# Kernel optimization log

Measured on AMD Instinct MI355X. Metric: run time of the kernel, lower is better.

## Reference

```python
import jax, jax.numpy as jnp
import numpy as np

B, T, C, WD = 8, 2048, 768, 512
TD, CD = 384, 3072   # tokens_dim=0.5*C, channels_dim=4*C
H1 = C               # default hidden of token StyleGLUs
EPS = 1e-6


def _ln(x, g, b):
    mu = jnp.mean(x, -1, keepdims=True)
    v = jnp.mean((x - mu) ** 2, -1, keepdims=True)
    return (x - mu) * jax.lax.rsqrt(v + EPS) * g + b


def _style_glu(x, w, gW, gb, sW, sb, mW, mb):
    # gate linear -> GLU -> style-modulated matmul (modulation folded into einsum)
    h = x @ gW + gb                       # [B,T,H]
    a, gt = jnp.split(h, 2, axis=-1)
    a = a * jax.nn.sigmoid(gt)            # [B,T,H/2]
    s = w @ sW + sb                       # [B,H/2] per-sample style scale
    return jnp.einsum('bth,bh,ho->bto', a, s, mW) + mb


def setup_inputs() -> dict:
    key = jax.random.key(0)
    ks = iter(jax.random.split(key, 40))
    def nrm(*s, sc=0.02):
        return jax.random.normal(next(ks), s, dtype=jnp.float32) * sc
    return dict(
        x=jax.random.normal(next(ks), (B, T, C), dtype=jnp.float32),
        w=jax.random.normal(next(ks), (B, 2, WD), dtype=jnp.float32),
        ln1_g=jnp.ones(C, jnp.float32), ln1_b=jnp.zeros(C, jnp.float32),
        ln2_g=jnp.ones(C, jnp.float32), ln2_b=jnp.zeros(C, jnp.float32),
        g1_W=nrm(C, H1), g1_b=jnp.zeros(H1, jnp.float32),
        s1_W=nrm(WD, H1 // 2), s1_b=jnp.zeros(H1 // 2, jnp.float32),
        m1_W=nrm(H1 // 2, TD, sc=0.05), m1_b=nrm(TD, sc=0.05),
        g2_W=nrm(C, H1), g2_b=jnp.zeros(H1, jnp.float32),
        s2_W=nrm(WD, H1 // 2), s2_b=jnp.zeros(H1 // 2, jnp.float32),
        m2_W=nrm(H1 // 2, TD, sc=0.05), m2_b=nrm(TD, sc=0.05),
        gs_W=nrm(C, CD), gs_b=jnp.zeros(CD, jnp.float32),
        ss_W=nrm(WD, CD // 2), ss_b=jnp.zeros(CD // 2, jnp.float32),
        ms_W=nrm(CD // 2, C, sc=0.05), ms_b=nrm(C, sc=0.05),
        r1_W=nrm(C, C), r1_b=jnp.zeros(C, jnp.float32),
        r2_W=nrm(C // 2, C), r2_b=jnp.zeros(C, jnp.float32),
    )


def reference(x, w, ln1_g, ln1_b, ln2_g, ln2_b,
              g1_W, g1_b, s1_W, s1_b, m1_W, m1_b,
              g2_W, g2_b, s2_W, s2_b, m2_W, m2_b,
              gs_W, gs_b, ss_W, ss_b, ms_W, ms_b,
              r1_W, r1_b, r2_W, r2_b):
    x = _ln(x, ln1_g, ln1_b)
    w0, w1 = w[:, 0], w[:, 1]
    # --- StyleHyperMixer token mixing (eval: dropout/droppath = identity) ---
    h1 = _style_glu(x, w0, g1_W, g1_b, s1_W, s1_b, m1_W, m1_b)  # [B,T,TD]
    h2 = _style_glu(x, w0, g2_W, g2_b, s2_W, s2_b, m2_W, m2_b)  # [B,T,TD]
    mix = jax.nn.gelu(jnp.einsum('btd,btc->bdc', h1, x), approximate=False)  # [B,TD,C]
    x = x + jnp.einsum('btd,bdc->btc', h2, mix)
    # --- style-modulated channel MLP ---
    x = x + _style_glu(_ln(x, ln2_g, ln2_b), w1, gs_W, gs_b, ss_W, ss_b, ms_W, ms_b)
    # --- GLU reduce ---
    h = x @ r1_W + r1_b
    a, gt = jnp.split(h, 2, axis=-1)
    return (a * jax.nn.sigmoid(gt)) @ r2_W + r2_b
```

## Files before the change

kernel.cpp:

```cpp
#include <hip/hip_runtime.h>
#include <hip/hip_bf16.h>
#include <math.h>

#define NB 8
#define NT 2048
#define NC 768
#define ROWS (NB*NT)

typedef __attribute__((ext_vector_type(8))) short s8v;
typedef __attribute__((ext_vector_type(4))) float f4v;

__device__ __forceinline__ unsigned short f2b(float f) {
    unsigned u = __builtin_bit_cast(unsigned, f);
    return (unsigned short)((u + 0x7FFFu + ((u >> 16) & 1u)) >> 16);
}

__device__ __forceinline__ void gll16(const ushort* g, ushort* l) {
    __builtin_amdgcn_global_load_lds(
        (const __attribute__((address_space(1))) void*)g,
        (__attribute__((address_space(3))) void*)l, 16, 0, 0);
}

template<int N> __device__ __forceinline__ void waitcnt_vm() {
    if constexpr (N == 3)      asm volatile("s_waitcnt vmcnt(3)" ::: "memory");
    else if constexpr (N == 4) asm volatile("s_waitcnt vmcnt(4)" ::: "memory");
    else if constexpr (N == 6) asm volatile("s_waitcnt vmcnt(6)" ::: "memory");
    else                       asm volatile("s_waitcnt vmcnt(0)" ::: "memory");
}
__device__ __forceinline__ void hw_barrier() {
    asm volatile("s_barrier" ::: "memory");
}

template<int R>
__device__ __forceinline__ void stageL(ushort* __restrict__ L, const ushort* __restrict__ G,
                                       int ld, int r0, int k0, int lane, int w) {
    int rs = lane >> 2, c = lane & 3;
#pragma unroll
    for (int i = 0; i < R / 64; i++) {
        int ii = w + 4 * i;
        int row = ii * 16 + rs;
        int kc = (c ^ ((row >> 1) & 3)) << 3;
        gll16(G + (long)(r0 + row) * ld + k0 + kc, L + ii * 512);
    }
}

template<int TN, int EPI, bool HASBIAS, bool SPLITK>
__global__ __launch_bounds__(256) void gemm_mfma(
    const ushort* __restrict__ A, const ushort* __restrict__ Bt,
    float* __restrict__ Cf, ushort* __restrict__ Cb,
    int M, int N, int K, int lda, int ldb, int ldc,
    long sA, long sB, long sC, const float* __restrict__ bias)
{
    constexpr int WM = (TN == 128) ? 64 : 32;
    constexpr int TI = WM / 16;
    constexpr int BN = TN * 32;
    constexpr int LP = 2 + TN / 64;
    int zz = blockIdx.z;
    int z  = SPLITK ? (zz >> 2) : zz;
    int kb = SPLITK ? (zz & 3) * (K >> 2) : 0;
    int ke = SPLITK ? kb + (K >> 2) : K;
    const ushort* Az = A + (long)z * sA;
    const ushort* Bz = Bt + (long)z * sB;
    float*  Cfz = Cf ? Cf + (long)z * sC : nullptr;
    ushort* Cbz = Cb ? Cb + (long)z * sC : nullptr;

    int m0 = blockIdx.y * 128, n0 = blockIdx.x * TN;
    __shared__ alignas(16) ushort Al[8192];
    __shared__ alignas(16) ushort Bl[2 * BN];
    int t = threadIdx.x;
    int lane = t & 63, w = t >> 6;
    int wm = (TN == 128) ? (w >> 1) * 64 : w * 32;
    int wn = (TN == 128) ? (w & 1) * 64 : 0;
    int fr = lane & 15, q = lane >> 4;

    f4v acc[TI][4];
#pragma unroll
    for (int i = 0; i < TI; i++)
#pragma unroll
        for (int j = 0; j < 4; j++) acc[i][j] = (f4v)(0.0f);

    auto frag_mfma = [&](const ushort* AB, const ushort* BB) {
        s8v af[TI], bf[4];
#pragma unroll
        for (int ti = 0; ti < TI; ti++) {
            int r = wm + ti * 16 + fr;
            af[ti] = *(const s8v*)&AB[r * 32 + ((q ^ ((r >> 1) & 3)) << 3)];
        }
#pragma unroll
        for (int tj = 0; tj < 4; tj++) {
            int r = wn + tj * 16 + fr;
            bf[tj] = *(const s8v*)&BB[r * 32 + ((q ^ ((r >> 1) & 3)) << 3)];
        }
#pragma unroll
        for (int ti = 0; ti < TI; ti++)
#pragma unroll
            for (int tj = 0; tj < 4; tj++)
                acc[ti][tj] = __builtin_amdgcn_mfma_f32_16x16x32_bf16(
                    af[ti], bf[tj], acc[ti][tj], 0, 0, 0);
    };

    int nt = (ke - kb) >> 5;
    stageL<128>(Al, Az, lda, m0, kb, lane, w);
    stageL<TN>(Bl, Bz, ldb, n0, kb, lane, w);
    int cur = 0;
    for (int it = 0; it + 1 < nt; ++it) {
        stageL<128>(Al + (cur ^ 1) * 4096, Az, lda, m0, kb + (it + 1) * 32, lane, w);
        stageL<TN>(Bl + (cur ^ 1) * BN, Bz, ldb, n0, kb + (it + 1) * 32, lane, w);
        waitcnt_vm<LP>();
        hw_barrier();
        frag_mfma(Al + cur * 4096, Bl + cur * BN);
        hw_barrier();
        cur ^= 1;
    }
    waitcnt_vm<0>();
    hw_barrier();
    frag_mfma(Al + cur * 4096, Bl + cur * BN);

    int cr0 = q * 4;
#pragma unroll
    for (int ti = 0; ti < TI; ti++) {
#pragma unroll
        for (int tj = 0; tj < 4; tj++) {
            int n = n0 + wn + tj * 16 + fr;
            float bv = HASBIAS ? bias[n] : 0.0f;
#pragma unroll
            for (int r = 0; r < 4; r++) {
                int m = m0 + wm + ti * 16 + cr0 + r;
                long idx = (long)m * ldc + n;
                float v = acc[ti][tj][r] + bv;
                if (EPI == 0) {
                    Cbz[idx] = f2b(v);
                } else if (EPI == 5) {
                    Cfz[idx] = v;
                } else if (EPI == 6) {
                    __hip_atomic_fetch_add(&Cfz[idx], v, __ATOMIC_RELAXED,
                                           __HIP_MEMORY_SCOPE_AGENT);
                } else {
                    v += Cfz[idx];
                    if (EPI == 3) Cfz[idx] = v;
                    if (EPI == 4) Cbz[idx] = f2b(v);
                }
            }
        }
    }
}

template<int TN, bool HAS_S>
__global__ __launch_bounds__(256) void gemm_glu_mfma(
    const ushort* __restrict__ A,
    const ushort* __restrict__ Bt0, const ushort* __restrict__ Bt1,
    ushort* __restrict__ C0, ushort* __restrict__ C1,
    int M, int Nh, int K, int lda,
    const float* __restrict__ bias0, const float* __restrict__ bias1,
    const float* __restrict__ s0, const float* __restrict__ s1, int bofs)
{
    constexpr int WM = (TN == 128) ? 64 : 32;
    constexpr int TI = WM / 16;
    constexpr int BN = TN * 32;
    constexpr int LP = 2 + 2 * (TN / 64);
    int z = blockIdx.z;
    const ushort* Bt = z ? Bt1 : Bt0;
    ushort* Cb = z ? C1 : C0;
    const float* bias = z ? bias1 : bias0;
    const float* s = z ? s1 : s0;

    int m0 = blockIdx.y * 128, n0 = blockIdx.x * TN;
    __shared__ alignas(16) ushort Al[8192];
    __shared__ alignas(16) ushort B1[2 * BN];
    __shared__ alignas(16) ushort B2[2 * BN];
    int t = threadIdx.x;
    int lane = t & 63, w = t >> 6;
    int wm = (TN == 128) ? (w >> 1) * 64 : w * 32;
    int wn = (TN == 128) ? (w & 1) * 64 : 0;
    int fr = lane & 15, q = lane >> 4;

    f4v acc1[TI][4], acc2[TI][4];
#pragma unroll
    for (int i = 0; i < TI; i++)
#pragma unroll
        for (int j = 0; j < 4; j++) { acc1[i][j] = (f4v)(0.0f); acc2[i][j] = (f4v)(0.0f); }

    auto frag_mfma = [&](const ushort* AB, const ushort* BB1, const ushort* BB2) {
        s8v af[TI], b1f[4], b2f[4];
#pragma unroll
        for (int ti = 0; ti < TI; ti++) {
            int r = wm + ti * 16 + fr;
            af[ti] = *(const s8v*)&AB[r * 32 + ((q ^ ((r >> 1) & 3)) << 3)];
        }
#pragma unroll
        for (int tj = 0; tj < 4; tj++) {
            int r = wn + tj * 16 + fr;
            int o = r * 32 + ((q ^ ((r >> 1) & 3)) << 3);
            b1f[tj] = *(const s8v*)&BB1[o];
            b2f[tj] = *(const s8v*)&BB2[o];
        }
#pragma unroll
        for (int ti = 0; ti < TI; ti++)
#pragma unroll
            for (int tj = 0; tj < 4; tj++) {
                acc1[ti][tj] = __builtin_amdgcn_mfma_f32_16x16x32_bf16(af[ti], b1f[tj], acc1[ti][tj], 0, 0, 0);
                acc2[ti][tj] = __builtin_amdgcn_mfma_f32_16x16x32_bf16(af[ti], b2f[tj], acc2[ti][tj], 0, 0, 0);
            }
    };

    int nt = K >> 5;
    stageL<TN>(B1, Bt, K, n0, 0, lane, w);
    stageL<TN>(B2, Bt, K, Nh + n0, 0, lane, w);
    stageL<128>(Al, A, lda, m0, 0, lane, w);
    int cur = 0;
    for (int it = 0; it + 1 < nt; ++it) {
        int k0 = (it + 1) * 32;
        stageL<TN>(B1 + (cur ^ 1) * BN, Bt, K, n0, k0, lane, w);
        stageL<TN>(B2 + (cur ^ 1) * BN, Bt, K, Nh + n0, k0, lane, w);
        stageL<128>(Al + (cur ^ 1) * 4096, A, lda, m0, k0, lane, w);
        waitcnt_vm<LP>();
        hw_barrier();
        frag_mfma(Al + cur * 4096, B1 + cur * BN, B2 + cur * BN);
        hw_barrier();
        cur ^= 1;
    }
    waitcnt_vm<0>();
    hw_barrier();
    frag_mfma(Al + cur * 4096, B1 + cur * BN, B2 + cur * BN);

    int cr0 = q * 4;
#pragma unroll
    for (int ti = 0; ti < TI; ti++) {
        int bb = ((m0 + wm + ti * 16 + cr0) >> 11) + bofs;
#pragma unroll
        for (int tj = 0; tj < 4; tj++) {
            int n = n0 + wn + tj * 16 + fr;
            float bv = bias[n], bg = bias[Nh + n];
            float sv = HAS_S ? s[(long)bb * Nh + n] : 1.0f;
#pragma unroll
            for (int r = 0; r < 4; r++) {
                int m = m0 + wm + ti * 16 + cr0 + r;
                float vv = acc1[ti][tj][r] + bv;
                float gg = acc2[ti][tj][r] + bg;
                float a = vv * (1.0f / (1.0f + __expf(-gg)));
                if (HAS_S) a *= sv;
                Cb[(long)m * Nh + n] = f2b(a);
            }
        }
    }
}

__global__ __launch_bounds__(256) void gelu_cast_kernel(const float* __restrict__ in,
                                                        ushort* __restrict__ out) {
    int i4 = (blockIdx.x * 256 + threadIdx.x) * 4;
    float4 v = *(const float4*)(in + i4);
    ushort4 o;
    o.x = f2b(0.5f * v.x * (1.0f + erff(v.x * 0.70710678118654752440f)));
    o.y = f2b(0.5f * v.y * (1.0f + erff(v.y * 0.70710678118654752440f)));
    o.z = f2b(0.5f * v.z * (1.0f + erff(v.z * 0.70710678118654752440f)));
    o.w = f2b(0.5f * v.w * (1.0f + erff(v.w * 0.70710678118654752440f)));
    *(ushort4*)(out + i4) = o;
}

template<bool SRC_F32>
__global__ __launch_bounds__(256) void transpose_kernel(const void* __restrict__ src,
                                                        ushort* __restrict__ dst,
                                                        int R, int C, long sS, long sD) {
    int z = blockIdx.z;
    const void* S = SRC_F32 ? (const void*)((const float*)src + (long)z * sS)
                            : (const void*)((const ushort*)src + (long)z * sS);
    ushort* D = dst + (long)z * sD;
    int r0 = blockIdx.y * 64, c0 = blockIdx.x * 64;
    __shared__ ushort T[64][68];
    int t = threadIdx.x;
#pragma unroll
    for (int p = 0; p < 4; p++) {
        int e = p * 256 + t;
        int row = e >> 4, cc = (e & 15) * 4;
        ushort4 v;
        if (SRC_F32) {
            float4 f = *(const float4*)((const float*)S + (long)(r0 + row) * C + c0 + cc);
            v.x = f2b(f.x); v.y = f2b(f.y); v.z = f2b(f.z); v.w = f2b(f.w);
        } else {
            v = *(const ushort4*)((const ushort*)S + (long)(r0 + row) * C + c0 + cc);
        }
        *(ushort4*)&T[row][cc] = v;
    }
    __syncthreads();
#pragma unroll
    for (int p = 0; p < 4; p++) {
        int e = p * 256 + t;
        int crow = e >> 4, rr = (e & 15) * 4;
        ushort4 o;
        o.x = T[rr + 0][crow]; o.y = T[rr + 1][crow];
        o.z = T[rr + 2][crow]; o.w = T[rr + 3][crow];
        *(ushort4*)&D[(long)(c0 + crow) * R + r0 + rr] = o;
    }
}

__global__ __launch_bounds__(256) void prep_kernel(
    const float* __restrict__ g1_W, ushort* __restrict__ g1t,
    const float* __restrict__ g2_W, ushort* __restrict__ g2t,
    const float* __restrict__ m1_W, ushort* __restrict__ m1t,
    const float* __restrict__ m2_W, ushort* __restrict__ m2t,
    const float* __restrict__ gs_W, ushort* __restrict__ gst,
    const float* __restrict__ ms_W, ushort* __restrict__ mst,
    const float* __restrict__ r1_W, ushort* __restrict__ r1t,
    const float* __restrict__ r2_W, ushort* __restrict__ r2t,
    const float* __restrict__ w,
    const float* __restrict__ s1W, const float* __restrict__ s1b,
    const float* __restrict__ s2W, const float* __restrict__ s2b,
    const float* __restrict__ ssW, const float* __restrict__ ssb,
    float* __restrict__ sout)
{
    int b = blockIdx.x, t = threadIdx.x;
    if (b < 23040) {
        const float* W; ushort* Wt; int K, N, lo;
        if      (b < 2304)  { W = g1_W; Wt = g1t; K = 768;  N = 768;  lo = 0; }
        else if (b < 4608)  { W = g2_W; Wt = g2t; K = 768;  N = 768;  lo = 2304; }
        else if (b < 5184)  { W = m1_W; Wt = m1t; K = 384;  N = 384;  lo = 4608; }
        else if (b < 5760)  { W = m2_W; Wt = m2t; K = 384;  N = 384;  lo = 5184; }
        else if (b < 14976) { W = gs_W; Wt = gst; K = 768;  N = 3072; lo = 5760; }
        else if (b < 19584) { W = ms_W; Wt = mst; K = 1536; N = 768;  lo = 14976; }
        else if (b < 21888) { W = r1_W; Wt = r1t; K = 768;  N = 768;  lo = 19584; }
        else                { W = r2_W; Wt = r2t; K = 384;  N = 768;  lo = 21888; }
        int local = b - lo, bx = K >> 6;
        int byi = local / bx, bxi = local - byi * bx;
        int k = bxi * 64 + (t & 63), n = byi * 4 + (t >> 6);
        Wt[(long)n * K + k] = f2b(W[(long)k * N + n]);
    } else {
        int gid = (b - 23040) * 256 + t;
        int bb = gid / 2304;
        int r  = gid % 2304;
        const float* w0 = w + (long)bb * 1024;
        const float* w1 = w0 + 512;
        float acc = 0.f;
        if (r < 384) {
            for (int k = 0; k < 512; k++) acc += w0[k] * s1W[k * 384 + r];
            sout[bb * 384 + r] = acc + s1b[r];
        } else if (r < 768) {
            int c = r - 384;
            for (int k = 0; k < 512; k++) acc += w0[k] * s2W[k * 384 + c];
            sout[3072 + bb * 384 + c] = acc + s2b[c];
        } else {
            int c = r - 768;
            for (int k = 0; k < 512; k++) acc += w1[k] * ssW[k * 1536 + c];
            sout[6144 + bb * 1536 + c] = acc + ssb[c];
        }
    }
}

template<int MODE>
__global__ __launch_bounds__(256) void ln_kernel(const float* __restrict__ x,
                                                 const float* __restrict__ g,
                                                 const float* __restrict__ b,
                                                 float* __restrict__ outf,
                                                 ushort* __restrict__ outb) {
    int row = blockIdx.x;
    const float* xr = x + (long)row * NC;
    int t = threadIdx.x;
    float v0 = xr[t], v1 = xr[t + 256], v2 = xr[t + 512];
    float s = v0 + v1 + v2;
    float s2 = v0 * v0 + v1 * v1 + v2 * v2;
    for (int off = 32; off > 0; off >>= 1) {
        s  += __shfl_down(s, off, 64);
        s2 += __shfl_down(s2, off, 64);
    }
    __shared__ float ls[4], ls2[4];
    int wid = t >> 6, lane = t & 63;
    if (lane == 0) { ls[wid] = s; ls2[wid] = s2; }
    __syncthreads();
    if (t == 0) {
        float ts = ls[0] + ls[1] + ls[2] + ls[3];
        float ts2 = ls2[0] + ls2[1] + ls2[2] + ls2[3];
        float mu = ts * (1.0f / NC);
        float var = ts2 * (1.0f / NC) - mu * mu;
        ls[0] = mu;
        ls2[0] = 1.0f / sqrtf(var + 1e-6f);
    }
    __syncthreads();
    float mu = ls[0], r = ls2[0];
#pragma unroll
    for (int i = 0; i < 3; i++) {
        int c = t + i * 256;
        float vv = (i == 0 ? v0 : (i == 1 ? v1 : v2));
        float o = (vv - mu) * r * g[c] + b[c];
        if (MODE == 2) outf[(long)row * NC + c] = o;
        outb[(long)row * NC + c] = f2b(o);
    }
}

extern "C" void kernel_launch(void* const* d_in, const int* in_sizes, int n_in,
                              void* d_out, int out_size, void* d_ws, size_t ws_size,
                              hipStream_t stream) {
    const float* x     = (const float*)d_in[0];
    const float* w     = (const float*)d_in[1];
    const float* ln1_g = (const float*)d_in[2];
    const float* ln1_b = (const float*)d_in[3];
    const float* ln2_g = (const float*)d_in[4];
    const float* ln2_b = (const float*)d_in[5];
    const float* g1_W  = (const float*)d_in[6];
    const float* g1_b  = (const float*)d_in[7];
    const float* s1_W  = (const float*)d_in[8];
    const float* s1_b  = (const float*)d_in[9];
    const float* m1_W  = (const float*)d_in[10];
    const float* m1_b  = (const float*)d_in[11];
    const float* g2_W  = (const float*)d_in[12];
    const float* g2_b  = (const float*)d_in[13];
    const float* s2_W  = (const float*)d_in[14];
    const float* s2_b  = (const float*)d_in[15];
    const float* m2_W  = (const float*)d_in[16];
    const float* m2_b  = (const float*)d_in[17];
    const float* gs_W  = (const float*)d_in[18];
    const float* gs_b  = (const float*)d_in[19];
    const float* ss_W  = (const float*)d_in[20];
    const float* ss_b  = (const float*)d_in[21];
    const float* ms_W  = (const float*)d_in[22];
    const float* ms_b  = (const float*)d_in[23];
    const float* r1_W  = (const float*)d_in[24];
    const float* r1_b  = (const float*)d_in[25];
    const float* r2_W  = (const float*)d_in[26];
    const float* r2_b  = (const float*)d_in[27];
    float* out = (float*)d_out;
    char* ws = (char*)d_ws;
    char* ob = (char*)d_out;

    float*  XLN = (float*)ws;
    ushort* A1b = (ushort*)(ws + 50331648);
    ushort* g1t = (ushort*)(ws + 62914560);
    ushort* g2t = g1t + 589824;
    ushort* m1t = g2t + 589824;
    ushort* m2t = m1t + 147456;
    ushort* gst = m2t + 147456;
    ushort* mst = gst + 2359296;
    ushort* r1t = mst + 1179648;
    ushort* r2t = r1t + 589824;
    float*  SV  = (float*)(ws + 74711040);
    ushort* H1T = A1b;
    ushort* ASq = A1b;
    ushort* ARq = A1b;

    ushort* XLNb  = (ushort*)(ob + 25165824);
    ushort* XLNT  = (ushort*)(ob + 25165824);
    ushort* A2q   = (ushort*)(ob + 12582912);
    ushort* H2q   = (ushort*)ob;
    ushort* H1q   = (ushort*)(ob + 12582912);
    float*  MIXTf = (float*)(ob + 12582912);
    ushort* MIXTb = (ushort*)(ob + 25165824);
    ushort* X2LNq = (ushort*)(ob + 25165824);
    ushort* X3q   = (ushort*)ob;

    prep_kernel<<<23112, 256, 0, stream>>>(
        g1_W, g1t, g2_W, g2t, m1_W, m1t, m2_W, m2t, gs_W, gst, ms_W, mst,
        r1_W, r1t, r2_W, r2t, w, s1_W, s1_b, s2_W, s2_b, ss_W, ss_b, SV);
    ln_kernel<2><<<ROWS, 256, 0, stream>>>(x, ln1_g, ln1_b, XLN, XLNb);

    gemm_glu_mfma<128, true><<<dim3(3, 128, 2), 256, 0, stream>>>(
        XLNb, g1t, g2t, A1b, A2q, ROWS, 384, 768, 768, g1_b, g2_b, SV, SV + 3072, 0);
    transpose_kernel<true><<<dim3(12, 32, NB), 256, 0, stream>>>(
        XLN, XLNT, 2048, 768, (long)2048 * 768, (long)768 * 2048);
    gemm_mfma<64, 0, true, false><<<dim3(6, 128), 256, 0, stream>>>(
        A2q, m2t, nullptr, H2q, ROWS, 384, 384, 384, 384, 384, 0, 0, 0, m2_b);
    gemm_mfma<64, 0, true, false><<<dim3(6, 128), 256, 0, stream>>>(
        A1b, m1t, nullptr, H1q, ROWS, 384, 384, 384, 384, 384, 0, 0, 0, m1_b);
    transpose_kernel<false><<<dim3(6, 32, NB), 256, 0, stream>>>(
        H1q, H1T, 2048, 384, (long)2048 * 384, (long)384 * 2048);
    hipMemsetAsync(MIXTf, 0, (size_t)NB * 768 * 384 * 4, stream);
    gemm_mfma<128, 6, false, true><<<dim3(3, 6, NB * 4), 256, 0, stream>>>(
        XLNT, H1T, MIXTf, nullptr, 768, 384, 2048, 2048, 2048, 384,
        (long)768 * 2048, (long)384 * 2048, (long)768 * 384, nullptr);
    gelu_cast_kernel<<<2304, 256, 0, stream>>>(MIXTf, MIXTb);
    gemm_mfma<128, 3, false, false><<<dim3(6, 16, NB), 256, 0, stream>>>(
        H2q, MIXTb, XLN, nullptr, 2048, 768, 384, 384, 384, 768,
        (long)2048 * 384, (long)768 * 384, (long)2048 * 768, nullptr);
    ln_kernel<1><<<ROWS, 256, 0, stream>>>(XLN, ln2_g, ln2_b, nullptr, X2LNq);
    for (int ch = 0; ch < 4; ch++) {
        ushort* X2c = X2LNq + (long)ch * 4096 * 768;
        float*  XLNc = XLN + (long)ch * 4096 * 768;
        ushort* X3c = X3q + (long)ch * 4096 * 768;
        gemm_glu_mfma<128, true><<<dim3(12, 32), 256, 0, stream>>>(
            X2c, gst, gst, ASq, ASq, 4096, 1536, 768, 768, gs_b, gs_b,
            SV + 6144, SV + 6144, ch * 2);
        gemm_mfma<128, 4, true, false><<<dim3(6, 32), 256, 0, stream>>>(
            ASq, mst, XLNc, X3c, 4096, 768, 1536, 1536, 1536, 768, 0, 0, 0, ms_b);
    }
    gemm_glu_mfma<64, false><<<dim3(6, 128), 256, 0, stream>>>(
        X3q, r1t, r1t, ARq, ARq, ROWS, 384, 768, 768, r1_b, r1_b, nullptr, nullptr, 0);
    gemm_mfma<128, 5, true, false><<<dim3(6, 128), 256, 0, stream>>>(
        ARq, r2t, out, nullptr, ROWS, 768, 384, 384, 384, 768, 0, 0, 0, r2_b);
}
```

Baseline: 830.8 us.

## Switch GEMM kernels to triple-buffered LDS pipeline with one barrier per step

Both GEMM kernels (plain and dual-B GLU) move from double-buffered LDS staging to a three-deep ring of buffers. Loads for tile k+2 are issued after the barrier, so two tiles are in flight while computing, and the trailing barrier per iteration is removed. The cost is 50% more LDS per block, which can lower occupancy, especially in the dual-B kernel.

```diff
diff --git a/kernel.cpp b/kernel.cpp
--- a/kernel.cpp
+++ b/kernel.cpp
@@ -65,8 +65,8 @@
     ushort* Cbz = Cb ? Cb + (long)z * sC : nullptr;
 
     int m0 = blockIdx.y * 128, n0 = blockIdx.x * TN;
-    __shared__ alignas(16) ushort Al[8192];
-    __shared__ alignas(16) ushort Bl[2 * BN];
+    __shared__ alignas(16) ushort Al[3 * 4096];
+    __shared__ alignas(16) ushort Bl[3 * BN];
     int t = threadIdx.x;
     int lane = t & 63, w = t >> 6;
     int wm = (TN == 128) ? (w >> 1) * 64 : w * 32;
@@ -100,21 +100,27 @@
     };
 
     int nt = (ke - kb) >> 5;
-    stageL<128>(Al, Az, lda, m0, kb, lane, w);
-    stageL<TN>(Bl, Bz, ldb, n0, kb, lane, w);
-    int cur = 0;
-    for (int it = 0; it + 1 < nt; ++it) {
-        stageL<128>(Al + (cur ^ 1) * 4096, Az, lda, m0, kb + (it + 1) * 32, lane, w);
-        stageL<TN>(Bl + (cur ^ 1) * BN, Bz, ldb, n0, kb + (it + 1) * 32, lane, w);
-        waitcnt_vm<LP>();
+    ushort *A0 = Al, *A1 = Al + 4096, *A2 = Al + 8192;
+    ushort *B0 = Bl, *B1 = Bl + BN,   *B2 = Bl + 2 * BN;
+    stageL<128>(A0, Az, lda, m0, kb, lane, w);
+    stageL<TN>(B0, Bz, ldb, n0, kb, lane, w);
+    if (nt > 1) {
+        stageL<128>(A1, Az, lda, m0, kb + 32, lane, w);
+        stageL<TN>(B1, Bz, ldb, n0, kb + 32, lane, w);
+    }
+    for (int it = 0; it < nt; ++it) {
+        if (it + 1 < nt) waitcnt_vm<LP>();
+        else             waitcnt_vm<0>();
         hw_barrier();
-        frag_mfma(Al + cur * 4096, Bl + cur * BN);
-        hw_barrier();
-        cur ^= 1;
-    }
-    waitcnt_vm<0>();
-    hw_barrier();
-    frag_mfma(Al + cur * 4096, Bl + cur * BN);
+        if (it + 2 < nt) {
+            stageL<128>(A2, Az, lda, m0, kb + (it + 2) * 32, lane, w);
+            stageL<TN>(B2, Bz, ldb, n0, kb + (it + 2) * 32, lane, w);
+        }
+        frag_mfma(A0, B0);
+        ushort* tp;
+        tp = A0; A0 = A1; A1 = A2; A2 = tp;
+        tp = B0; B0 = B1; B1 = B2; B2 = tp;
+    }
 
     int cr0 = q * 4;
 #pragma unroll
@@ -165,9 +171,9 @@
     const float* s = z ? s1 : s0;
 
     int m0 = blockIdx.y * 128, n0 = blockIdx.x * TN;
-    __shared__ alignas(16) ushort Al[8192];
-    __shared__ alignas(16) ushort B1[2 * BN];
-    __shared__ alignas(16) ushort B2[2 * BN];
+    __shared__ alignas(16) ushort Al[3 * 4096];
+    __shared__ alignas(16) ushort Bu[3 * BN];
+    __shared__ alignas(16) ushort Bv[3 * BN];
     int t = threadIdx.x;
     int lane = t & 63, w = t >> 6;
     int wm = (TN == 128) ? (w >> 1) * 64 : w * 32;
@@ -204,24 +210,33 @@
     };
 
     int nt = K >> 5;
-    stageL<TN>(B1, Bt, K, n0, 0, lane, w);
-    stageL<TN>(B2, Bt, K, Nh + n0, 0, lane, w);
-    stageL<128>(Al, A, lda, m0, 0, lane, w);
-    int cur = 0;
-    for (int it = 0; it + 1 < nt; ++it) {
-        int k0 = (it + 1) * 32;
-        stageL<TN>(B1 + (cur ^ 1) * BN, Bt, K, n0, k0, lane, w);
-        stageL<TN>(B2 + (cur ^ 1) * BN, Bt, K, Nh + n0, k0, lane, w);
-        stageL<128>(Al + (cur ^ 1) * 4096, A, lda, m0, k0, lane, w);
-        waitcnt_vm<LP>();
+    ushort *A0 = Al, *A1 = Al + 4096, *A2 = Al + 8192;
+    ushort *U0 = Bu, *U1 = Bu + BN,   *U2 = Bu + 2 * BN;
+    ushort *V0 = Bv, *V1 = Bv + BN,   *V2 = Bv + 2 * BN;
+    stageL<TN>(U0, Bt, K, n0, 0, lane, w);
+    stageL<TN>(V0, Bt, K, Nh + n0, 0, lane, w);
+    stageL<128>(A0, A, lda, m0, 0, lane, w);
+    if (nt > 1) {
+        stageL<TN>(U1, Bt, K, n0, 32, lane, w);
+        stageL<TN>(V1, Bt, K, Nh + n0, 32, lane, w);
+        stageL<128>(A1, A, lda, m0, 32, lane, w);
+    }
+    for (int it = 0; it < nt; ++it) {
+        if (it + 1 < nt) waitcnt_vm<LP>();
+        else             waitcnt_vm<0>();
         hw_barrier();
-        frag_mfma(Al + cur * 4096, B1 + cur * BN, B2 + cur * BN);
-        hw_barrier();
-        cur ^= 1;
-    }
-    waitcnt_vm<0>();
-    hw_barrier();
-    frag_mfma(Al + cur * 4096, B1 + cur * BN, B2 + cur * BN);
+        if (it + 2 < nt) {
+            int k0 = (it + 2) * 32;
+            stageL<TN>(U2, Bt, K, n0, k0, lane, w);
+            stageL<TN>(V2, Bt, K, Nh + n0, k0, lane, w);
+            stageL<128>(A2, A, lda, m0, k0, lane, w);
+        }
+        frag_mfma(A0, U0, V0);
+        ushort* tp;
+        tp = A0; A0 = A1; A1 = A2; A2 = tp;
+        tp = U0; U0 = U1; U1 = U2; U2 = tp;
+        tp = V0; V0 = V1; V1 = V2; V2 = tp;
+    }
 
     int cr0 = q * 4;
 #pragma unroll
```

Result: slower. 880.7 us (+6.0%).
